# Kernel optimization log

Hardware: AMD Instinct MI355X
Metric: run time of the kernel (lower is better)

## Reference

```python
import jax, jax.numpy as jnp
import numpy as np

N, IN, HID, OUT, G = 1_000_000, 128, 64, 1, 10_000


def setup_inputs() -> dict:
    key = jax.random.key(0)
    k1, k2, k3, k4 = jax.random.split(key, 4)
    H = jax.random.normal(k1, (N, IN), dtype=jnp.float32)
    # glorot-ish init scale for the small MLP weights
    w1 = jax.random.normal(k2, (HID, IN), dtype=jnp.float32) * (1.0 / np.sqrt(IN))
    w2 = jax.random.normal(k3, (OUT, HID), dtype=jnp.float32) * (1.0 / np.sqrt(HID))
    batch = jnp.sort(jax.random.randint(k4, (N,), 0, G, dtype=jnp.int32)).astype(jnp.int64)
    return {"H": H, "w1": w1, "w2": w2, "batch": batch, "size": G}


def reference(H, w1, w2, batch, size):
    # x = tanh(w1 @ H^T) ; scores = w2 @ x  -> written row-major: [N, out]
    x = jnp.tanh(H @ w1.T)          # [N, hid]
    s = x @ w2.T                    # [N, out]
    # segment (per-graph) softmax over nodes
    m = jax.ops.segment_max(s, batch, num_segments=size)      # [G, out]
    m = jnp.where(jnp.isfinite(m), m, 0.0)                    # guard empty segments
    e = jnp.exp(s - m[batch])                                 # [N, out]
    denom = jax.ops.segment_sum(e, batch, num_segments=size)  # [G, out]
    S = e / denom[batch]                                      # [N, out], out==1
    # scatter_add(S * H, batch, dim_size=size)
    fin_x = jax.ops.segment_sum(S * H, batch, num_segments=size)  # [G, in]
    return fin_x
```

## Files before the change

kernel.cpp:

```cpp
#include <hip/hip_runtime.h>
#include <hip/hip_bf16.h>
#include <math.h>

#define IN_DIM 128
#define HID_DIM 64

typedef __attribute__((ext_vector_type(8))) short short8;
typedef __attribute__((ext_vector_type(4))) float floatx4;

__device__ __forceinline__ short f2bf(float f) {
    unsigned u = __float_as_uint(f);
    u += 0x7FFFu + ((u >> 16) & 1u);
    return (short)(u >> 16);
}

__device__ __forceinline__ short8 pack_bf16(float4 f0, float4 f1) {
    short8 r;
    r[0] = f2bf(f0.x); r[1] = f2bf(f0.y); r[2] = f2bf(f0.z); r[3] = f2bf(f0.w);
    r[4] = f2bf(f1.x); r[5] = f2bf(f1.y); r[6] = f2bf(f1.z); r[7] = f2bf(f1.w);
    return r;
}

__device__ __forceinline__ float fast_tanh(float x) {
    float ax = fabsf(x);
    float z  = __expf(-2.0f * ax);
    float t  = (1.0f - z) * __builtin_amdgcn_rcpf(1.0f + z);
    return copysignf(t, x);
}

extern "C" __global__ __launch_bounds__(256, 3) void k_score(
    const float* __restrict__ H, const float* __restrict__ w1,
    const float* __restrict__ w2, float* __restrict__ e_arr, int n)
{
    const int wave = threadIdx.x >> 6;
    const int lane = threadIdx.x & 63;
    const int col  = lane & 15;
    const int quad = lane >> 4;
    const int base = (blockIdx.x * 4 + wave) * 64;

    short8 bf[4][4];
    {
        const float* wb = w1 + (size_t)col * IN_DIM + quad * 8;
#pragma unroll
        for (int t = 0; t < 4; ++t) {
            const float* wt = wb + t * 16 * IN_DIM;
#pragma unroll
            for (int c = 0; c < 4; ++c) {
                float4 f0 = *(const float4*)(wt + c * 32);
                float4 f1 = *(const float4*)(wt + c * 32 + 4);
                bf[t][c] = pack_bf16(f0, f1);
            }
        }
    }

    floatx4 acc[4][4];
#pragma unroll
    for (int mt = 0; mt < 4; ++mt)
#pragma unroll
        for (int t = 0; t < 4; ++t)
            acc[mt][t] = (floatx4){0.f, 0.f, 0.f, 0.f};

    const float* hrow[4];
#pragma unroll
    for (int mt = 0; mt < 4; ++mt) {
        int node = base + mt * 16 + col;
        if (node >= n) node = n - 1;
        hrow[mt] = H + (size_t)node * IN_DIM + quad * 8;
    }

#pragma unroll
    for (int c = 0; c < 4; ++c) {
#pragma unroll
        for (int mt = 0; mt < 4; ++mt) {
            float4 f0 = *(const float4*)(hrow[mt] + c * 32);
            float4 f1 = *(const float4*)(hrow[mt] + c * 32 + 4);
            short8 a = pack_bf16(f0, f1);
#pragma unroll
            for (int t = 0; t < 4; ++t)
                acc[mt][t] = __builtin_amdgcn_mfma_f32_16x16x32_bf16(
                    a, bf[t][c], acc[mt][t], 0, 0, 0);
        }
    }

    float w2v[4];
#pragma unroll
    for (int t = 0; t < 4; ++t) w2v[t] = w2[t * 16 + col];

#pragma unroll
    for (int mt = 0; mt < 4; ++mt) {
        float s[4];
#pragma unroll
        for (int r = 0; r < 4; ++r) {
            float p = 0.f;
#pragma unroll
            for (int t = 0; t < 4; ++t)
                p = fmaf(w2v[t], fast_tanh(acc[mt][t][r]), p);
            p += __shfl_xor(p, 1);
            p += __shfl_xor(p, 2);
            p += __shfl_xor(p, 4);
            p += __shfl_xor(p, 8);
            s[r] = p;
        }
        if (col == 0) {
            int node4 = base + mt * 16 + quad * 4;
            if (node4 + 3 < n) {
                float4 ev = make_float4(__expf(s[0]), __expf(s[1]),
                                        __expf(s[2]), __expf(s[3]));
                *(float4*)(e_arr + node4) = ev;
            } else {
#pragma unroll
                for (int r = 0; r < 4; ++r)
                    if (node4 + r < n) e_arr[node4 + r] = __expf(s[r]);
            }
        }
    }
}

extern "C" __global__ __launch_bounds__(256) void k_accum(
    const float* __restrict__ H, const int* __restrict__ batch,
    const float* __restrict__ e_arr, float* __restrict__ out, int n, int G)
{
    int g    = (int)((blockIdx.x * 256 + threadIdx.x) >> 5);
    int lane = threadIdx.x & 31;
    if (g >= G) return;

    int lo = 0, hi = n;
    while (lo < hi) { int mid = (lo + hi) >> 1; if (batch[mid] < g) lo = mid + 1; else hi = mid; }
    int lo2 = lo, hi2 = n;
    while (lo2 < hi2) { int mid = (lo2 + hi2) >> 1; if (batch[mid] < g + 1) lo2 = mid + 1; else hi2 = mid; }
    int cnt = lo2 - lo;

    const float* hp = H + (size_t)lo * IN_DIM + lane * 4;
    const float* ep = e_arr + lo;

    float4 acc = make_float4(0.f, 0.f, 0.f, 0.f);
    float esum = 0.f;

    int t = 0;
    for (; t + 8 <= cnt; t += 8) {
        float4 hb[8];
        float  eb[8];
#pragma unroll
        for (int u = 0; u < 8; ++u) {
            hb[u] = *(const float4*)(hp + (size_t)(t + u) * IN_DIM);
            eb[u] = ep[t + u];
        }
#pragma unroll
        for (int u = 0; u < 8; ++u) {
            acc.x = fmaf(eb[u], hb[u].x, acc.x);
            acc.y = fmaf(eb[u], hb[u].y, acc.y);
            acc.z = fmaf(eb[u], hb[u].z, acc.z);
            acc.w = fmaf(eb[u], hb[u].w, acc.w);
            esum += eb[u];
        }
    }
    for (; t < cnt; ++t) {
        float4 h = *(const float4*)(hp + (size_t)t * IN_DIM);
        float  e = ep[t];
        acc.x = fmaf(e, h.x, acc.x);
        acc.y = fmaf(e, h.y, acc.y);
        acc.z = fmaf(e, h.z, acc.z);
        acc.w = fmaf(e, h.w, acc.w);
        esum += e;
    }

    float inv = (esum != 0.f) ? 1.0f / esum : 0.f;
    float4 o = make_float4(acc.x * inv, acc.y * inv, acc.z * inv, acc.w * inv);
    *(float4*)(out + (size_t)g * IN_DIM + lane * 4) = o;
}

extern "C" void kernel_launch(void* const* d_in, const int* in_sizes, int n_in,
                              void* d_out, int out_size, void* d_ws, size_t ws_size,
                              hipStream_t stream)
{
    const float* H     = (const float*)d_in[0];
    const float* w1    = (const float*)d_in[1];
    const float* w2    = (const float*)d_in[2];
    const int*   batch = (const int*)d_in[3];
    float*       out   = (float*)d_out;

    int n = in_sizes[0] / IN_DIM;
    int G = out_size / IN_DIM;

    float* e_arr = (float*)d_ws;

    int blocks1 = (n + 255) / 256;
    k_score<<<blocks1, 256, 0, stream>>>(H, w1, w2, e_arr, n);

    int blocks2 = (G * 32 + 255) / 256;
    k_accum<<<blocks2, 256, 0, stream>>>(H, batch, e_arr, out, n, G);
}
```

Before: 780.8 us.

## Fuse score and segment accumulation into one per-graph wave kernel

Replaces the two-kernel pipeline (score kernel writing exp-scores to a workspace, then a per-graph accumulation kernel) with a single kernel in which each wave owns one graph. The wave runs the bf16 MFMA MLP over its graph's rows 16 at a time, broadcasts the exp-scores across lanes, and accumulates the weighted H rows into the output. The aim is to avoid reading H twice from HBM (the second read is expected to hit cache) and to drop the workspace round-trip and one launch. In exchange, per-graph segments of about 100 rows give uneven work per wave and partially filled 16-row tiles, and each lane now loads only a float2 per row in the accumulation step.

```diff
diff --git a/kernel.cpp b/kernel.cpp
--- a/kernel.cpp
+++ b/kernel.cpp
@@ -1,5 +1,4 @@
 #include <hip/hip_runtime.h>
-#include <hip/hip_bf16.h>
 #include <math.h>
 
 #define IN_DIM 128
@@ -28,15 +27,31 @@
     return copysignf(t, x);
 }
 
-extern "C" __global__ __launch_bounds__(256, 3) void k_score(
+extern "C" __global__ __launch_bounds__(256, 3) void k_fused(
     const float* __restrict__ H, const float* __restrict__ w1,
-    const float* __restrict__ w2, float* __restrict__ e_arr, int n)
+    const float* __restrict__ w2, const int* __restrict__ batch,
+    float* __restrict__ out, int n, int G)
 {
     const int wave = threadIdx.x >> 6;
     const int lane = threadIdx.x & 63;
     const int col  = lane & 15;
     const int quad = lane >> 4;
-    const int base = (blockIdx.x * 4 + wave) * 64;
+    const int g    = blockIdx.x * 4 + wave;
+    if (g >= G) return;
+
+    int lo = 0, hi = n;
+    while (lo < hi) { int mid = (lo + hi) >> 1; if (batch[mid] < g) lo = mid + 1; else hi = mid; }
+    int lo2 = lo, hi2 = n;
+    while (lo2 < hi2) { int mid = (lo2 + hi2) >> 1; if (batch[mid] < g + 1) lo2 = mid + 1; else hi2 = mid; }
+    const int cnt = lo2 - lo;
+
+    float* og = out + (size_t)g * IN_DIM;
+    const int d0 = lane * 2;
+
+    if (cnt == 0) {
+        *(float2*)(og + d0) = make_float2(0.f, 0.f);
+        return;
+    }
 
     short8 bf[4][4];
     {
@@ -52,121 +67,74 @@
             }
         }
     }
-
-    floatx4 acc[4][4];
-#pragma unroll
-    for (int mt = 0; mt < 4; ++mt)
-#pragma unroll
-        for (int t = 0; t < 4; ++t)
-            acc[mt][t] = (floatx4){0.f, 0.f, 0.f, 0.f};
-
-    const float* hrow[4];
-#pragma unroll
-    for (int mt = 0; mt < 4; ++mt) {
-        int node = base + mt * 16 + col;
-        if (node >= n) node = n - 1;
-        hrow[mt] = H + (size_t)node * IN_DIM + quad * 8;
-    }
-
-#pragma unroll
-    for (int c = 0; c < 4; ++c) {
-#pragma unroll
-        for (int mt = 0; mt < 4; ++mt) {
-            float4 f0 = *(const float4*)(hrow[mt] + c * 32);
-            float4 f1 = *(const float4*)(hrow[mt] + c * 32 + 4);
-            short8 a = pack_bf16(f0, f1);
-#pragma unroll
-            for (int t = 0; t < 4; ++t)
-                acc[mt][t] = __builtin_amdgcn_mfma_f32_16x16x32_bf16(
-                    a, bf[t][c], acc[mt][t], 0, 0, 0);
-        }
-    }
-
     float w2v[4];
 #pragma unroll
     for (int t = 0; t < 4; ++t) w2v[t] = w2[t * 16 + col];
 
+    float accx = 0.f, accy = 0.f, esum = 0.f;
+
+    for (int t0 = 0; t0 < cnt; t0 += 16) {
+        const int rem = cnt - t0;
+
+        int row = t0 + col;
+        if (row >= cnt) row = cnt - 1;
+        const float* hr = H + (size_t)(lo + row) * IN_DIM + quad * 8;
+
+        floatx4 acc[4];
 #pragma unroll
-    for (int mt = 0; mt < 4; ++mt) {
-        float s[4];
+        for (int t = 0; t < 4; ++t) acc[t] = (floatx4){0.f, 0.f, 0.f, 0.f};
+
+#pragma unroll
+        for (int c = 0; c < 4; ++c) {
+            float4 f0 = *(const float4*)(hr + c * 32);
+            float4 f1 = *(const float4*)(hr + c * 32 + 4);
+            short8 a = pack_bf16(f0, f1);
+#pragma unroll
+            for (int t = 0; t < 4; ++t)
+                acc[t] = __builtin_amdgcn_mfma_f32_16x16x32_bf16(
+                    a, bf[t][c], acc[t], 0, 0, 0);
+        }
+
+        float e4[4];
 #pragma unroll
         for (int r = 0; r < 4; ++r) {
             float p = 0.f;
 #pragma unroll
             for (int t = 0; t < 4; ++t)
-                p = fmaf(w2v[t], fast_tanh(acc[mt][t][r]), p);
+                p = fmaf(w2v[t], fast_tanh(acc[t][r]), p);
             p += __shfl_xor(p, 1);
             p += __shfl_xor(p, 2);
             p += __shfl_xor(p, 4);
             p += __shfl_xor(p, 8);
-            s[r] = p;
+            e4[r] = __expf(p);
         }
-        if (col == 0) {
-            int node4 = base + mt * 16 + quad * 4;
-            if (node4 + 3 < n) {
-                float4 ev = make_float4(__expf(s[0]), __expf(s[1]),
-                                        __expf(s[2]), __expf(s[3]));
-                *(float4*)(e_arr + node4) = ev;
-            } else {
+
+        float e_all[16];
 #pragma unroll
-                for (int r = 0; r < 4; ++r)
-                    if (node4 + r < n) e_arr[node4 + r] = __expf(s[r]);
-            }
+        for (int r = 0; r < 4; ++r)
+#pragma unroll
+            for (int q = 0; q < 4; ++q)
+                e_all[q * 4 + r] = __shfl(e4[r], q * 16);
+
+#pragma unroll
+        for (int j = 0; j < 16; ++j) {
+            if (j >= rem) e_all[j] = 0.f;
+            esum += e_all[j];
+        }
+
+        const int m = rem < 16 ? rem : 16;
+        const float* hb = H + (size_t)(lo + t0) * IN_DIM + d0;
+#pragma unroll
+        for (int j = 0; j < 16; ++j) {
+            int jr = j < m ? j : m - 1;
+            float2 h = *(const float2*)(hb + (size_t)jr * IN_DIM);
+            accx = fmaf(e_all[j], h.x, accx);
+            accy = fmaf(e_all[j], h.y, accy);
         }
     }
-}
 
-extern "C" __global__ __launch_bounds__(256) void k_accum(
-    const float* __restrict__ H, const int* __restrict__ batch,
-    const float* __restrict__ e_arr, float* __restrict__ out, int n, int G)
-{
-    int g    = (int)((blockIdx.x * 256 + threadIdx.x) >> 5);
-    int lane = threadIdx.x & 31;
-    if (g >= G) return;
-
-    int lo = 0, hi = n;
-    while (lo < hi) { int mid = (lo + hi) >> 1; if (batch[mid] < g) lo = mid + 1; else hi = mid; }
-    int lo2 = lo, hi2 = n;
-    while (lo2 < hi2) { int mid = (lo2 + hi2) >> 1; if (batch[mid] < g + 1) lo2 = mid + 1; else hi2 = mid; }
-    int cnt = lo2 - lo;
-
-    const float* hp = H + (size_t)lo * IN_DIM + lane * 4;
-    const float* ep = e_arr + lo;
-
-    float4 acc = make_float4(0.f, 0.f, 0.f, 0.f);
-    float esum = 0.f;
-
-    int t = 0;
-    for (; t + 8 <= cnt; t += 8) {
-        float4 hb[8];
-        float  eb[8];
-#pragma unroll
-        for (int u = 0; u < 8; ++u) {
-            hb[u] = *(const float4*)(hp + (size_t)(t + u) * IN_DIM);
-            eb[u] = ep[t + u];
-        }
-#pragma unroll
-        for (int u = 0; u < 8; ++u) {
-            acc.x = fmaf(eb[u], hb[u].x, acc.x);
-            acc.y = fmaf(eb[u], hb[u].y, acc.y);
-            acc.z = fmaf(eb[u], hb[u].z, acc.z);
-            acc.w = fmaf(eb[u], hb[u].w, acc.w);
-            esum += eb[u];
-        }
-    }
-    for (; t < cnt; ++t) {
-        float4 h = *(const float4*)(hp + (size_t)t * IN_DIM);
-        float  e = ep[t];
-        acc.x = fmaf(e, h.x, acc.x);
-        acc.y = fmaf(e, h.y, acc.y);
-        acc.z = fmaf(e, h.z, acc.z);
-        acc.w = fmaf(e, h.w, acc.w);
-        esum += e;
-    }
-
-    float inv = (esum != 0.f) ? 1.0f / esum : 0.f;
-    float4 o = make_float4(acc.x * inv, acc.y * inv, acc.z * inv, acc.w * inv);
-    *(float4*)(out + (size_t)g * IN_DIM + lane * 4) = o;
+    const float inv = 1.0f / esum;
+    *(float2*)(og + d0) = make_float2(accx * inv, accy * inv);
 }
 
 extern "C" void kernel_launch(void* const* d_in, const int* in_sizes, int n_in,
@@ -182,11 +150,6 @@
     int n = in_sizes[0] / IN_DIM;
     int G = out_size / IN_DIM;
 
-    float* e_arr = (float*)d_ws;
-
-    int blocks1 = (n + 255) / 256;
-    k_score<<<blocks1, 256, 0, stream>>>(H, w1, w2, e_arr, n);
-
-    int blocks2 = (G * 32 + 255) / 256;
-    k_accum<<<blocks2, 256, 0, stream>>>(H, batch, e_arr, out, n, G);
+    int blocks = (G + 3) / 4;
+    k_fused<<<blocks, 256, 0, stream>>>(H, w1, w2, batch, out, n, G);
 }
```

Measured after the change: 723.3 us. 1.08x faster.
